# Performance work log

Measured on AMD Instinct MI355X. Metric: run time of the kernel, lower is better.

The kernel has to match this reference:

```python
import jax, jax.numpy as jnp
import numpy as np

# dims
B, N = 8, 16384
MODEL_DIM = 256
F = 32        # feature_dim
H = 4         # num_heads
G = 32        # grid_size
G3 = G * G * G
EPS = 1e-5


def setup_inputs() -> dict:
    key = jax.random.key(0)
    ks = jax.random.split(key, 9)
    eye = jnp.broadcast_to(jnp.eye(3, dtype=jnp.float32), (H, 3, 3))
    return {
        "input_tensor": jax.random.normal(ks[0], (B, MODEL_DIM, N), dtype=jnp.float32),
        "original_points": jax.random.normal(ks[1], (B, 3, N), dtype=jnp.float32),
        # Conv1d kernel_size=1, no bias -> plain (out,in) matmul weight
        "W_kv": jax.random.normal(ks[2], (H * (F + 3), MODEL_DIM), dtype=jnp.float32) * 0.02,
        # key BN affine (orig init weight=0; use small random to exercise path)
        "key_gamma": jax.random.normal(ks[3], (H * 3,), dtype=jnp.float32) * 0.1,
        "key_beta": jax.random.normal(ks[4], (H * 3,), dtype=jnp.float32) * 0.1,
        "val_gamma": 1.0 + jax.random.normal(ks[5], (H * F,), dtype=jnp.float32) * 0.1,
        "val_beta": jax.random.normal(ks[6], (H * F,), dtype=jnp.float32) * 0.1,
        # VolTransformer: per-head affine (rotation-ish matrix + translation)
        "R": eye + jax.random.normal(ks[7], (H, 3, 3), dtype=jnp.float32) * 0.05,
        "t": jax.random.normal(ks[8], (H, 3), dtype=jnp.float32) * 0.1,
    }


def _bn(x, gamma, beta):
    # training-mode BatchNorm1d over (batch, length) per channel; x: (B, C, N)
    mean = jnp.mean(x, axis=(0, 2), keepdims=True)
    var = jnp.var(x, axis=(0, 2), keepdims=True)
    xhat = (x - mean) * jax.lax.rsqrt(var + EPS)
    return xhat * gamma[None, :, None] + beta[None, :, None]


def reference(input_tensor, original_points, W_kv, key_gamma, key_beta,
              val_gamma, val_beta, R, t):
    # 1x1 conv == channel matmul: (B, H*(F+3), N)
    kv = jnp.einsum('om,bmn->bon', W_kv, input_tensor)
    keys_offset = _bn(kv[:, :H * 3], key_gamma, key_beta)          # (B, H*3, N)
    values = _bn(kv[:, H * 3:], val_gamma, val_beta)               # (B, H*F, N)

    keys_offset = keys_offset.reshape(B, H, 3, N)
    pts = original_points[:, None, :, :] + keys_offset             # (B,H,3,N)
    # per-head affine transform (VolTransformer)
    tk = jnp.einsum('hij,bhjn->bhin', R, pts) + t[None, :, :, None]
    lattice = jnp.tanh(tk)                                         # in (-1,1)

    # DifferentiablePositions: map (-1,1) -> [0, G-1], lower corner + local frac
    pos = (lattice + 1.0) * (0.5 * (G - 1))                        # (B,H,3,N)
    idx0 = jnp.clip(jnp.floor(pos), 0.0, G - 2).astype(jnp.int32)  # (B,H,3,N)
    local = pos - idx0                                             # (B,H,3,N)

    values_t = values.reshape(B, H, F, N).transpose(0, 1, 3, 2)    # (B,H,N,F)
    bh_off = (jnp.arange(B * H, dtype=jnp.int32).reshape(B, H) * G3)[:, :, None]

    out = jnp.zeros((B * H * G3, F), dtype=values.dtype)
    # trilinear splat-scatter over the 8 grid corners
    for cx in (0, 1):
        wx = local[:, :, 0] if cx else 1.0 - local[:, :, 0]
        for cy in (0, 1):
            wy = local[:, :, 1] if cy else 1.0 - local[:, :, 1]
            for cz in (0, 1):
                wz = local[:, :, 2] if cz else 1.0 - local[:, :, 2]
                w = wx * wy * wz                                    # (B,H,N)
                flat = ((idx0[:, :, 0] + cx) * G + (idx0[:, :, 1] + cy)) * G \
                       + (idx0[:, :, 2] + cz)                       # (B,H,N)
                seg = (bh_off + flat).reshape(-1)                   # (B*H*N,)
                data = (values_t * w[..., None]).reshape(-1, F)
                out = out + jax.ops.segment_sum(data, seg, num_segments=B * H * G3)

    # (B, H*F, G, G, G)
    return out.reshape(B, H, G3, F).transpose(0, 1, 3, 2).reshape(B, H * F, G, G, G)
```

## Files before the change

kernel.cpp:

```cpp
#include <hip/hip_runtime.h>
#include <hip/hip_bf16.h>
#include <cstddef>

#define Bz 8
#define Nn 16384
#define MD 256
#define Ff 32
#define Hh 4
#define Gg 32
#define G3v 32768
#define CKV 140
#define NG 32
#define NBX 31
#define NBY 31
#define NBZ 31
#define NB2 953312
#define NCH 931

using bf16x8 = __attribute__((ext_vector_type(8))) short;
using f32x16 = __attribute__((ext_vector_type(16))) float;

__device__ __forceinline__ unsigned bf16rne(float f) {
    unsigned u = __float_as_uint(f);
    return (u + 0x7fffu + ((u >> 16) & 1u)) >> 16;
}
__device__ __forceinline__ unsigned cvt2(float lo, float hi) {
    __hip_bfloat162 hb = __float22bfloat162_rn(make_float2(lo, hi));
    union { __hip_bfloat162 b; unsigned u; } c;
    c.b = hb;
    return c.u;
}

__global__ __launch_bounds__(256) void prep_w_kernel(const float* __restrict__ W,
                                                     unsigned short* __restrict__ Wbf)
{
    const int idx = blockIdx.x * 256 + threadIdx.x;
    const int e    = idx & 7;
    const int rest = idx >> 3;
    const int m    = rest % 160;
    const int kg   = rest / 160;
    const int k    = (kg << 3) + e;
    Wbf[idx] = (m < CKV) ? (unsigned short)bf16rne(W[m * MD + k]) : (unsigned short)0;
}

__global__ __launch_bounds__(256, 3) void gemm_stats_kernel(
    const float* __restrict__ X, const unsigned short* __restrict__ Wbf,
    float* __restrict__ vals, float* __restrict__ keys,
    float* __restrict__ gsum, float* __restrict__ gsq)
{
    __shared__ float smem[9216];
    __shared__ float red[280];
    unsigned* XlU = reinterpret_cast<unsigned*>(smem);
    unsigned* WlU = reinterpret_cast<unsigned*>(smem) + 4096;

    const int bid = blockIdx.x;
    const int b   = bid >> 7;
    const int n0  = (bid & 127) << 7;
    const int t   = threadIdx.x;
    const int w   = t >> 6;
    const int ln  = t & 31;
    const int hi  = (t >> 5) & 1;

    f32x16 acc[5];
    #pragma unroll
    for (int mt = 0; mt < 5; ++mt)
        #pragma unroll
        for (int j = 0; j < 16; ++j) acc[mt][j] = 0.f;

    for (int ks = 0; ks < 4; ++ks) {
        const int k0 = ks << 6;
        if (ks > 0) __syncthreads();

        #pragma unroll
        for (int it = 0; it < 4; ++it) {
            const int a  = t + (it << 8);
            const int kp = a >> 5;
            const int n4 = (a & 31) << 2;
            const float4 r0 = *reinterpret_cast<const float4*>(
                X + (size_t)(b * MD + k0 + 2 * kp) * Nn + n0 + n4);
            const float4 r1 = *reinterpret_cast<const float4*>(
                X + (size_t)(b * MD + k0 + 2 * kp + 1) * Nn + n0 + n4);
            const int base = ((kp >> 2) << 9) + (n4 << 2) + (kp & 3);
            XlU[base]      = cvt2(r0.x, r1.x);
            XlU[base + 4]  = cvt2(r0.y, r1.y);
            XlU[base + 8]  = cvt2(r0.z, r1.z);
            XlU[base + 12] = cvt2(r0.w, r1.w);
        }
        {
            const unsigned* src = reinterpret_cast<const unsigned*>(Wbf) + ks * 5120;
            #pragma unroll
            for (int i = 0; i < 5; ++i) {
                const int d4 = (t + (i << 8)) << 2;
                *reinterpret_cast<uint4*>(&WlU[d4]) =
                    *reinterpret_cast<const uint4*>(&src[d4]);
            }
        }
        __syncthreads();

        const short* xs = reinterpret_cast<const short*>(XlU);
        const short* ws = reinterpret_cast<const short*>(WlU);
        #pragma unroll
        for (int kk = 0; kk < 4; ++kk) {
            const int grp = (kk << 1) + hi;
            const bf16x8 bf = *reinterpret_cast<const bf16x8*>(
                xs + (((grp << 7) + (w << 5) + ln) << 3));
            #pragma unroll
            for (int mt = 0; mt < 5; ++mt) {
                const bf16x8 af = *reinterpret_cast<const bf16x8*>(
                    ws + ((grp * 160 + (mt << 5) + ln) << 3));
                acc[mt] = __builtin_amdgcn_mfma_f32_32x32x16_bf16(af, bf, acc[mt], 0, 0, 0);
            }
        }
    }

    const int n = n0 + (w << 5) + ln;
    #pragma unroll
    for (int reg = 0; reg < 8; ++reg) {
        const int ml = (reg & 3) + ((reg >> 2) << 3) + (hi << 2);
        if (ml < 12) {
            const int hh = ml / 3, kk2 = ml - (ml / 3) * 3;
            keys[(size_t)((b * Hh + hh) * 3 + kk2) * Nn + n] = acc[0][reg];
        }
    }

    const int nl = (w << 5) + ln;
    #pragma unroll
    for (int mt = 0; mt < 5; ++mt) {
        __syncthreads();
        #pragma unroll
        for (int reg = 0; reg < 16; ++reg) {
            const int ml = (reg & 3) + ((reg >> 2) << 3) + (hi << 2);
            smem[nl * 36 + ml] = acc[mt][reg];
        }
        __syncthreads();
        #pragma unroll
        for (int i = 0; i < 4; ++i) {
            const int id = t + (i << 8);
            const int nn = id >> 3;
            const int q  = id & 7;
            const int c  = (mt << 5) + (q << 2);
            if (c < 12 || c >= CKV) continue;
            const int cv = c - 12;
            const float4 v4 = *reinterpret_cast<const float4*>(&smem[nn * 36 + (q << 2)]);
            *reinterpret_cast<float4*>(
                &vals[((size_t)(b * Hh + (cv >> 5)) * Nn + n0 + nn) * Ff + (cv & 31)]) = v4;
        }
    }

    red[t] = 0.f;
    if (t < 24) red[256 + t] = 0.f;
    __syncthreads();
    #pragma unroll
    for (int mt = 0; mt < 5; ++mt)
        #pragma unroll
        for (int reg = 0; reg < 16; ++reg) {
            if (mt == 4 && reg >= 8) continue;
            const int ml = (reg & 3) + ((reg >> 2) << 3) + (hi << 2);
            const int c  = mt * 32 + ml;
            float s = acc[mt][reg];
            float q = s * s;
            #pragma unroll
            for (int off = 1; off < 32; off <<= 1) {
                s += __shfl_xor(s, off);
                q += __shfl_xor(q, off);
            }
            if (ln == 0 && c < CKV) {
                atomicAdd(&red[c], s);
                atomicAdd(&red[140 + c], q);
            }
        }
    __syncthreads();
    if (t < CKV) {
        atomicAdd(&gsum[t], red[t]);
        atomicAdd(&gsq[t],  red[140 + t]);
    }
}

__global__ void finalize_kernel(const float* __restrict__ gsum, const float* __restrict__ gsq,
                                const float* __restrict__ kg, const float* __restrict__ kb,
                                const float* __restrict__ vg, const float* __restrict__ vb,
                                float* __restrict__ scale, float* __restrict__ shift)
{
    const int c = threadIdx.x;
    if (c < CKV) {
        const float inv = 1.f / (float)(Bz * Nn);
        const float m = gsum[c] * inv;
        const float v = fmaf(-m, m, gsq[c] * inv);
        float ga, be;
        if (c < 12) { ga = kg[c]; be = kb[c]; }
        else        { ga = vg[c - 12]; be = vb[c - 12]; }
        const float sc = ga * rsqrtf(v + 1e-5f);
        scale[c] = sc;
        shift[c] = fmaf(-m, sc, be);
    }
}

__global__ __launch_bounds__(256) void points_kernel(
    const float* __restrict__ keys, const float* __restrict__ orig,
    const float* __restrict__ Rm, const float* __restrict__ tv,
    const float* __restrict__ scale, const float* __restrict__ shift,
    float4* __restrict__ rec, int* __restrict__ cnt)
{
    const int bid = blockIdx.x;
    const int g   = bid >> 6;
    const int b   = g >> 2;
    const int h   = g & 3;
    const int t   = threadIdx.x;
    const int n   = ((bid & 63) << 8) + t;

    __shared__ float sR[9], st3[3], ksc[3], ksh[3];
    if (t < 9)       sR[t] = Rm[h * 9 + t];
    else if (t < 12) st3[t - 9] = tv[h * 3 + (t - 9)];
    else if (t < 15) { ksc[t - 12] = scale[h * 3 + (t - 12)];
                       ksh[t - 12] = shift[h * 3 + (t - 12)]; }
    __syncthreads();

    const float k0 = fmaf(keys[(size_t)(g * 3 + 0) * Nn + n], ksc[0], ksh[0]);
    const float k1 = fmaf(keys[(size_t)(g * 3 + 1) * Nn + n], ksc[1], ksh[1]);
    const float k2 = fmaf(keys[(size_t)(g * 3 + 2) * Nn + n], ksc[2], ksh[2]);
    const float p0 = orig[(size_t)(b * 3 + 0) * Nn + n] + k0;
    const float p1 = orig[(size_t)(b * 3 + 1) * Nn + n] + k1;
    const float p2 = orig[(size_t)(b * 3 + 2) * Nn + n] + k2;

    int   idx[3];
    float loc[3];
    #pragma unroll
    for (int d = 0; d < 3; ++d) {
        const float tk = fmaf(sR[d*3+0], p0, fmaf(sR[d*3+1], p1, fmaf(sR[d*3+2], p2, st3[d])));
        const float la = tanhf(tk);
        const float po = (la + 1.f) * 15.5f;
        float fi = floorf(po);
        fi = fminf(fmaxf(fi, 0.f), 30.f);
        idx[d] = (int)fi;
        loc[d] = po - fi;
    }

    const unsigned meta = (unsigned)n | ((unsigned)idx[2] << 14) |
                          ((unsigned)idx[1] << 19) | ((unsigned)idx[0] << 24);
    float4 r;
    r.x = __uint_as_float(meta);
    r.y = loc[0]; r.z = loc[1]; r.w = loc[2];
    rec[(size_t)g * Nn + n] = r;
    const int key = ((g * NBX + idx[0]) * NBY + idx[1]) * NBZ + idx[2];
    atomicAdd(&cnt[key], 1);
}

__global__ __launch_bounds__(256) void scan1_kernel(const int* __restrict__ cnt,
                                                    int* __restrict__ bsum)
{
    __shared__ int s[256];
    const int t = threadIdx.x;
    const int i = blockIdx.x * 1024 + t * 4;
    int v = 0;
    #pragma unroll
    for (int j = 0; j < 4; ++j) { const int idx = i + j; if (idx < NB2) v += cnt[idx]; }
    s[t] = v;
    __syncthreads();
    for (int off = 128; off > 0; off >>= 1) {
        if (t < off) s[t] += s[t + off];
        __syncthreads();
    }
    if (t == 0) bsum[blockIdx.x] = s[0];
}

__global__ __launch_bounds__(1024) void scan2_kernel(const int* __restrict__ bsum,
                                                     int* __restrict__ bscan)
{
    __shared__ int s[1024];
    const int t = threadIdx.x;
    const int v = (t < NCH) ? bsum[t] : 0;
    s[t] = v;
    __syncthreads();
    for (int off = 1; off < 1024; off <<= 1) {
        const int x = (t >= off) ? s[t - off] : 0;
        __syncthreads();
        s[t] += x;
        __syncthreads();
    }
    if (t < NCH) bscan[t] = s[t] - v;
}

__global__ __launch_bounds__(256) void scan3_kernel(const int* __restrict__ cnt,
                                                    const int* __restrict__ bscan,
                                                    int* __restrict__ basep,
                                                    int* __restrict__ cursor)
{
    __shared__ int s[256];
    const int t = threadIdx.x;
    const int i = blockIdx.x * 1024 + t * 4;
    int c[4], l[4];
    int sum = 0;
    #pragma unroll
    for (int j = 0; j < 4; ++j) {
        const int idx = i + j;
        c[j] = (idx < NB2) ? cnt[idx] : 0;
        l[j] = sum; sum += c[j];
    }
    s[t] = sum;
    __syncthreads();
    for (int off = 1; off < 256; off <<= 1) {
        const int x = (t >= off) ? s[t - off] : 0;
        __syncthreads();
        s[t] += x;
        __syncthreads();
    }
    const int off0 = bscan[blockIdx.x] + s[t] - sum;
    #pragma unroll
    for (int j = 0; j < 4; ++j) {
        const int idx = i + j;
        if (idx < NB2) { basep[idx] = off0 + l[j]; cursor[idx] = off0 + l[j]; }
    }
}

__global__ __launch_bounds__(256) void fill_kernel(
    const float4* __restrict__ rec, int* __restrict__ cursor,
    float4* __restrict__ binned)
{
    const int bid = blockIdx.x;
    const int g   = bid >> 6;
    const int t   = threadIdx.x;
    const int n   = ((bid & 63) << 8) + t;
    const float4 r = rec[(size_t)g * Nn + n];
    const unsigned meta = __float_as_uint(r.x);
    const int x0 = (meta >> 24) & 31;
    const int y0 = (meta >> 19) & 31;
    const int z0 = (meta >> 14) & 31;
    const int key = ((g * NBX + x0) * NBY + y0) * NBZ + z0;
    const int pos = atomicAdd(&cursor[key], 1);
    binned[pos] = r;
}

#define MKAB(qe, ridx, ae, ve)                                               \
{                                                                            \
    const unsigned mq = __float_as_uint((qe).x);                             \
    const int z0 = (int)((mq >> 14) & 31u);                                  \
    const float wx  = dx ? (1.f - (qe).y) : (qe).y;                          \
    const float wy  = dy ? (1.f - (qe).z) : (qe).z;                          \
    const float wxy = ((ridx) < e) ? wx * wy : 0.f;                          \
    const float lz  = (qe).w;                                                \
    ae = (ln == z0) ? (1.f - lz) * wxy                                       \
                    : ((ln == z0 + 1) ? lz * wxy : 0.f);                     \
    ve = fmaf(vg[(((size_t)(mq & 16383u)) << 5) + ln], scf, shf);            \
}

__global__ __launch_bounds__(1024) void gather_kernel(
    const float* __restrict__ vals, const float4* __restrict__ binned,
    const int* __restrict__ basep, const int* __restrict__ cnt,
    const float* __restrict__ scale, const float* __restrict__ shift,
    float* __restrict__ out)
{
    __shared__ float tile[16384];
    __shared__ float sscale[32], sshift[32];

    const int bid = blockIdx.x;
    const int g   = bid & 31;
    const int x   = (bid >> 5) & 31;
    const int yh  = bid >> 10;
    const int h   = g & 3;
    const int t   = threadIdx.x;

    if (t < 32) { sscale[t] = scale[12 + h * 32 + t]; sshift[t] = shift[12 + h * 32 + t]; }
    __syncthreads();

    const int ln = t & 31;
    const int hi = (t >> 5) & 1;
    const int w  = t >> 6;
    const int y  = (yh << 4) + w;
    const float scf = sscale[ln], shf = sshift[ln];
    const float* vg = vals + ((size_t)g << 19);

    f32x16 acc;
    #pragma unroll
    for (int j = 0; j < 16; ++j) acc[j] = 0.f;

    #pragma unroll
    for (int dy = 0; dy < 2; ++dy) {
        const int y0 = y - 1 + dy;
        if ((unsigned)y0 > 30u) continue;
        #pragma unroll
        for (int dx = 0; dx < 2; ++dx) {
            const int x0 = x - 1 + dx;
            if ((unsigned)x0 > 30u) continue;
            const int kb = ((g * NBX + x0) * NBY + y0) * NBZ;
            int r       = basep[kb];
            const int e = basep[kb + 30] + cnt[kb + 30];

            for (; r < e; r += 16) {
                const int base = r + (hi << 3);
                const int eM1  = e - 1;
                const int r0 = min(base,     eM1);
                const int r1 = min(base + 1, eM1);
                const int r2 = min(base + 2, eM1);
                const int r3 = min(base + 3, eM1);
                const int r4 = min(base + 4, eM1);
                const int r5 = min(base + 5, eM1);
                const int r6 = min(base + 6, eM1);
                const int r7 = min(base + 7, eM1);
                const float4 q0 = binned[r0];
                const float4 q1 = binned[r1];
                const float4 q2 = binned[r2];
                const float4 q3 = binned[r3];
                const float4 q4 = binned[r4];
                const float4 q5 = binned[r5];
                const float4 q6 = binned[r6];
                const float4 q7 = binned[r7];
                float a0, a1, a2, a3, a4, a5, a6, a7;
                float v0, v1, v2, v3, v4, v5, v6, v7;
                MKAB(q0, base,     a0, v0);
                MKAB(q1, base + 1, a1, v1);
                MKAB(q2, base + 2, a2, v2);
                MKAB(q3, base + 3, a3, v3);
                MKAB(q4, base + 4, a4, v4);
                MKAB(q5, base + 5, a5, v5);
                MKAB(q6, base + 6, a6, v6);
                MKAB(q7, base + 7, a7, v7);
                union { bf16x8 v; unsigned u[4]; } af, bf;
                af.u[0] = cvt2(a0, a1); af.u[1] = cvt2(a2, a3);
                af.u[2] = cvt2(a4, a5); af.u[3] = cvt2(a6, a7);
                bf.u[0] = cvt2(v0, v1); bf.u[1] = cvt2(v2, v3);
                bf.u[2] = cvt2(v4, v5); bf.u[3] = cvt2(v6, v7);
                acc = __builtin_amdgcn_mfma_f32_32x32x16_bf16(af.v, bf.v, acc, 0, 0, 0);
            }
        }
    }

    float* const tg = &tile[w << 10];
    #pragma unroll
    for (int reg = 0; reg < 16; ++reg) {
        const int zr = (reg & 3) + ((reg >> 2) << 3) + (hi << 2);
        tg[(zr << 5) + ((ln ^ zr) & 31)] = acc[reg];
    }
    __syncthreads();

    float* og = out + ((size_t)g << 20) + (x << 10) + (yh << 9);
    #pragma unroll
    for (int i = 0; i < 16; ++i) {
        const int lin = t + (i << 10);
        const int fp  = lin >> 9;
        const int s   = lin & 511;
        const int z   = s & 31;
        og[((size_t)fp << 15) + s] = tile[((s >> 5) << 10) + (z << 5) + ((fp ^ z) & 31)];
    }
}

__global__ __launch_bounds__(256) void scatter_kernel(
    const float* __restrict__ vals, const float* __restrict__ keys,
    const float* __restrict__ orig, const float* __restrict__ Rm,
    const float* __restrict__ tv, const float* __restrict__ scale,
    const float* __restrict__ shift, float* __restrict__ out)
{
    const int bid   = blockIdx.x;
    const int g     = bid >> 5;
    const int chunk = bid & 31;
    const int b     = g >> 2;
    const int h     = g & 3;

    __shared__ float sc[32], sh[32], sR[9], st3[3], ksc[3], ksh[3];
    const int t = threadIdx.x;
    if (t < 32)      { sc[t] = scale[12 + h * 32 + t]; sh[t] = shift[12 + h * 32 + t]; }
    else if (t < 41) { sR[t - 32]  = Rm[h * 9 + (t - 32)]; }
    else if (t < 44) { st3[t - 41] = tv[h * 3 + (t - 41)]; }
    else if (t < 47) { ksc[t - 44] = scale[h * 3 + (t - 44)];
                       ksh[t - 44] = shift[h * 3 + (t - 44)]; }
    __syncthreads();

    float* const og = out + ((size_t)g << 20);

    #pragma unroll
    for (int pp = 0; pp < 2; ++pp) {
        const int n = (chunk << 9) + (pp << 8) + t;

        const float k0 = fmaf(keys[(size_t)(g * 3 + 0) * Nn + n], ksc[0], ksh[0]);
        const float k1 = fmaf(keys[(size_t)(g * 3 + 1) * Nn + n], ksc[1], ksh[1]);
        const float k2 = fmaf(keys[(size_t)(g * 3 + 2) * Nn + n], ksc[2], ksh[2]);
        const float p0 = orig[(size_t)(b * 3 + 0) * Nn + n] + k0;
        const float p1 = orig[(size_t)(b * 3 + 1) * Nn + n] + k1;
        const float p2 = orig[(size_t)(b * 3 + 2) * Nn + n] + k2;

        int   idx[3];
        float loc[3];
        #pragma unroll
        for (int d = 0; d < 3; ++d) {
            const float tk = fmaf(sR[d*3+0], p0, fmaf(sR[d*3+1], p1, fmaf(sR[d*3+2], p2, st3[d])));
            const float la = tanhf(tk);
            const float po = (la + 1.f) * 15.5f;
            float fi = floorf(po);
            fi = fminf(fmaxf(fi, 0.f), 30.f);
            idx[d] = (int)fi;
            loc[d] = po - fi;
        }
        const int cell = (idx[0] * Gg + idx[1]) * Gg + idx[2];

        float v[32];
        const float4* vp = reinterpret_cast<const float4*>(vals + ((size_t)g * Nn + n) * Ff);
        #pragma unroll
        for (int q = 0; q < 8; ++q) {
            const float4 xq = vp[q];
            v[4*q+0] = fmaf(xq.x, sc[4*q+0], sh[4*q+0]);
            v[4*q+1] = fmaf(xq.y, sc[4*q+1], sh[4*q+1]);
            v[4*q+2] = fmaf(xq.z, sc[4*q+2], sh[4*q+2]);
            v[4*q+3] = fmaf(xq.w, sc[4*q+3], sh[4*q+3]);
        }

        const float wx1 = loc[0], wx0 = 1.f - loc[0];
        const float wy1 = loc[1], wy0 = 1.f - loc[1];
        const float wz1 = loc[2], wz0 = 1.f - loc[2];
        const float cw[8] = { wx0*wy0*wz0, wx0*wy0*wz1, wx0*wy1*wz0, wx0*wy1*wz1,
                              wx1*wy0*wz0, wx1*wy0*wz1, wx1*wy1*wz0, wx1*wy1*wz1 };
        const int  co[8] = { 0, 1, 32, 33, 1024, 1025, 1056, 1057 };

        #pragma unroll
        for (int ff = 0; ff < 32; ++ff) {
            float* const pf = og + (size_t)ff * G3v + cell;
            const float vf = v[ff];
            #pragma unroll
            for (int c8 = 0; c8 < 8; ++c8) {
                atomicAdd(pf + co[c8], cw[c8] * vf);
            }
        }
    }
}

extern "C" void kernel_launch(void* const* d_in, const int* in_sizes, int n_in,
                              void* d_out, int out_size, void* d_ws, size_t ws_size,
                              hipStream_t stream)
{
    const float* X    = (const float*)d_in[0];
    const float* orig = (const float*)d_in[1];
    const float* W    = (const float*)d_in[2];
    const float* kg   = (const float*)d_in[3];
    const float* kb   = (const float*)d_in[4];
    const float* vg   = (const float*)d_in[5];
    const float* vb   = (const float*)d_in[6];
    const float* Rm   = (const float*)d_in[7];
    const float* tv   = (const float*)d_in[8];
    float* out = (float*)d_out;
    float* ws  = (float*)d_ws;

    float* vals  = ws;
    float* keys  = ws + 16777216;
    float* gsum  = ws + 18350080;
    float* gsq   = gsum + 140;
    float* scale = gsum + 280;
    float* shift = scale + 140;
    int*   cnt    = (int*)(ws + 18350848);
    int*   basep  = (int*)(ws + 19304160);
    int*   cursor = (int*)(ws + 20257472);
    int*   bsum   = (int*)(ws + 21210784);
    int*   bscan  = (int*)(ws + 21211808);
    float4* rec    = (float4*)(ws + 21212832);
    float4* binned = (float4*)(ws + 23309984);
    unsigned short* Wbf = (unsigned short*)(ws + 25407136);
    const size_t need_bytes = (size_t)25427616 * sizeof(float);

    hipMemsetAsync(gsum, 0, 280 * sizeof(float), stream);

    prep_w_kernel<<<160, 256, 0, stream>>>(W, Wbf);
    gemm_stats_kernel<<<1024, 256, 0, stream>>>(X, Wbf, vals, keys, gsum, gsq);
    finalize_kernel<<<1, 256, 0, stream>>>(gsum, gsq, kg, kb, vg, vb, scale, shift);

    if (ws_size >= need_bytes) {
        hipMemsetAsync(cnt, 0, (size_t)NB2 * sizeof(int), stream);
        points_kernel<<<2048, 256, 0, stream>>>(keys, orig, Rm, tv, scale, shift, rec, cnt);
        scan1_kernel<<<NCH, 256, 0, stream>>>(cnt, bsum);
        scan2_kernel<<<1, 1024, 0, stream>>>(bsum, bscan);
        scan3_kernel<<<NCH, 256, 0, stream>>>(cnt, bscan, basep, cursor);
        fill_kernel<<<2048, 256, 0, stream>>>(rec, cursor, binned);
        gather_kernel<<<2048, 1024, 0, stream>>>(vals, binned, basep, cnt, scale, shift, out);
    } else {
        hipMemsetAsync(out, 0, (size_t)out_size * sizeof(float), stream);
        scatter_kernel<<<1024, 256, 0, stream>>>(vals, keys, orig, Rm, tv, scale, shift, out);
    }
}
```

Measured before the change: 286.5 us.

## Split BN statistics out of GEMM and read weights directly from global

Drops the in-GEMM BatchNorm sum and sum-of-squares reduction (shuffles plus shared and global atomics) and moves it into two new kernels that re-read the keys and values buffers. The GEMM also stops staging the bf16 weight tile in LDS and loads MFMA A-fragments straight from global memory, which halves shared memory use and may raise occupancy. The cost is an extra full pass over the 64 MB values buffer, two more launches, and uncoalesced or L2-dependent weight loads inside the MFMA loop.

After: 282.6 us. Within noise of the previous version (-1.4%).

```diff
diff --git a/kernel.cpp b/kernel.cpp
--- a/kernel.cpp
+++ b/kernel.cpp
@@ -45,13 +45,10 @@
 
 __global__ __launch_bounds__(256, 3) void gemm_stats_kernel(
     const float* __restrict__ X, const unsigned short* __restrict__ Wbf,
-    float* __restrict__ vals, float* __restrict__ keys,
-    float* __restrict__ gsum, float* __restrict__ gsq)
-{
-    __shared__ float smem[9216];
-    __shared__ float red[280];
+    float* __restrict__ vals, float* __restrict__ keys)
+{
+    __shared__ float smem[4608];
     unsigned* XlU = reinterpret_cast<unsigned*>(smem);
-    unsigned* WlU = reinterpret_cast<unsigned*>(smem) + 4096;
 
     const int bid = blockIdx.x;
     const int b   = bid >> 7;
@@ -86,19 +83,10 @@
             XlU[base + 8]  = cvt2(r0.z, r1.z);
             XlU[base + 12] = cvt2(r0.w, r1.w);
         }
-        {
-            const unsigned* src = reinterpret_cast<const unsigned*>(Wbf) + ks * 5120;
-            #pragma unroll
-            for (int i = 0; i < 5; ++i) {
-                const int d4 = (t + (i << 8)) << 2;
-                *reinterpret_cast<uint4*>(&WlU[d4]) =
-                    *reinterpret_cast<const uint4*>(&src[d4]);
-            }
-        }
         __syncthreads();
 
         const short* xs = reinterpret_cast<const short*>(XlU);
-        const short* ws = reinterpret_cast<const short*>(WlU);
+        const short* wsg = reinterpret_cast<const short*>(Wbf) + (k0 << 7) * 5;
         #pragma unroll
         for (int kk = 0; kk < 4; ++kk) {
             const int grp = (kk << 1) + hi;
@@ -107,7 +95,8 @@
             #pragma unroll
             for (int mt = 0; mt < 5; ++mt) {
                 const bf16x8 af = *reinterpret_cast<const bf16x8*>(
-                    ws + ((grp * 160 + (mt << 5) + ln) << 3));
+                    reinterpret_cast<const short*>(Wbf) +
+                    ((((k0 >> 3) + grp) * 160 + (mt << 5) + ln) << 3));
                 acc[mt] = __builtin_amdgcn_mfma_f32_32x32x16_bf16(af, bf, acc[mt], 0, 0, 0);
             }
         }
@@ -146,33 +135,75 @@
                 &vals[((size_t)(b * Hh + (cv >> 5)) * Nn + n0 + nn) * Ff + (cv & 31)]) = v4;
         }
     }
-
-    red[t] = 0.f;
-    if (t < 24) red[256 + t] = 0.f;
-    __syncthreads();
-    #pragma unroll
-    for (int mt = 0; mt < 5; ++mt)
-        #pragma unroll
-        for (int reg = 0; reg < 16; ++reg) {
-            if (mt == 4 && reg >= 8) continue;
-            const int ml = (reg & 3) + ((reg >> 2) << 3) + (hi << 2);
-            const int c  = mt * 32 + ml;
-            float s = acc[mt][reg];
-            float q = s * s;
-            #pragma unroll
-            for (int off = 1; off < 32; off <<= 1) {
-                s += __shfl_xor(s, off);
-                q += __shfl_xor(q, off);
-            }
-            if (ln == 0 && c < CKV) {
-                atomicAdd(&red[c], s);
-                atomicAdd(&red[140 + c], q);
-            }
-        }
-    __syncthreads();
-    if (t < CKV) {
-        atomicAdd(&gsum[t], red[t]);
-        atomicAdd(&gsq[t],  red[140 + t]);
+}
+
+__global__ __launch_bounds__(256) void stats_keys_kernel(
+    const float* __restrict__ keys, float* __restrict__ gsum, float* __restrict__ gsq)
+{
+    const int g = blockIdx.x;
+    const int t = threadIdx.x;
+    __shared__ float rs[6];
+    if (t < 6) rs[t] = 0.f;
+    __syncthreads();
+    #pragma unroll
+    for (int kk = 0; kk < 3; ++kk) {
+        const float* p = keys + (size_t)(g * 3 + kk) * Nn;
+        float s = 0.f, q = 0.f;
+        for (int i = t * 4; i < Nn; i += 1024) {
+            const float4 v = *reinterpret_cast<const float4*>(p + i);
+            s += v.x + v.y + v.z + v.w;
+            q += v.x * v.x + v.y * v.y + v.z * v.z + v.w * v.w;
+        }
+        #pragma unroll
+        for (int off = 1; off < 64; off <<= 1) { s += __shfl_xor(s, off); q += __shfl_xor(q, off); }
+        if ((t & 63) == 0) { atomicAdd(&rs[kk], s); atomicAdd(&rs[3 + kk], q); }
+    }
+    __syncthreads();
+    if (t < 3) {
+        atomicAdd(&gsum[(g & 3) * 3 + t], rs[t]);
+        atomicAdd(&gsq[(g & 3) * 3 + t],  rs[3 + t]);
+    }
+}
+
+__global__ __launch_bounds__(256) void stats_vals_kernel(
+    const float* __restrict__ vals, float* __restrict__ gsum, float* __restrict__ gsq)
+{
+    const int bid   = blockIdx.x;
+    const int g     = bid >> 5;
+    const int chunk = bid & 31;
+    const int h     = g & 3;
+    const int t     = threadIdx.x;
+    const int fq    = t & 7;
+    const int nl    = t >> 3;
+    __shared__ float red[64];
+    if (t < 64) red[t] = 0.f;
+    __syncthreads();
+
+    float s0 = 0, s1 = 0, s2 = 0, s3 = 0, q0 = 0, q1 = 0, q2 = 0, q3 = 0;
+    const float* base = vals + ((size_t)g * Nn + chunk * 512) * Ff + fq * 4;
+    #pragma unroll
+    for (int i = 0; i < 16; ++i) {
+        const float4 v = *reinterpret_cast<const float4*>(base + (size_t)(nl + i * 32) * Ff);
+        s0 += v.x; s1 += v.y; s2 += v.z; s3 += v.w;
+        q0 += v.x * v.x; q1 += v.y * v.y; q2 += v.z * v.z; q3 += v.w * v.w;
+    }
+    #pragma unroll
+    for (int off = 8; off < 64; off <<= 1) {
+        s0 += __shfl_xor(s0, off); s1 += __shfl_xor(s1, off);
+        s2 += __shfl_xor(s2, off); s3 += __shfl_xor(s3, off);
+        q0 += __shfl_xor(q0, off); q1 += __shfl_xor(q1, off);
+        q2 += __shfl_xor(q2, off); q3 += __shfl_xor(q3, off);
+    }
+    if ((t & 56) == 0) {
+        atomicAdd(&red[fq * 4 + 0], s0); atomicAdd(&red[fq * 4 + 1], s1);
+        atomicAdd(&red[fq * 4 + 2], s2); atomicAdd(&red[fq * 4 + 3], s3);
+        atomicAdd(&red[32 + fq * 4 + 0], q0); atomicAdd(&red[32 + fq * 4 + 1], q1);
+        atomicAdd(&red[32 + fq * 4 + 2], q2); atomicAdd(&red[32 + fq * 4 + 3], q3);
+    }
+    __syncthreads();
+    if (t < 32) {
+        atomicAdd(&gsum[12 + h * 32 + t], red[t]);
+        atomicAdd(&gsq[12 + h * 32 + t],  red[32 + t]);
     }
 }
 
@@ -556,7 +587,9 @@
     hipMemsetAsync(gsum, 0, 280 * sizeof(float), stream);
 
     prep_w_kernel<<<160, 256, 0, stream>>>(W, Wbf);
-    gemm_stats_kernel<<<1024, 256, 0, stream>>>(X, Wbf, vals, keys, gsum, gsq);
+    gemm_stats_kernel<<<1024, 256, 0, stream>>>(X, Wbf, vals, keys);
+    stats_keys_kernel<<<32, 256, 0, stream>>>(keys, gsum, gsq);
+    stats_vals_kernel<<<1024, 256, 0, stream>>>(vals, gsum, gsq);
     finalize_kernel<<<1, 256, 0, stream>>>(gsum, gsq, kg, kb, vg, vb, scale, shift);
 
     if (ws_size >= need_bytes) {
```
